# Kernel optimization log

Hardware: AMD Instinct MI355X
Metric: run time of the kernel (lower is better)

Reference implementation:

```python
import jax, jax.numpy as jnp
import numpy as np

N = 50000; F = 128; H = 128; E = 800000; G = 512; C = 1000; CE = 64; L = 128
EPS = 1e-5

def gcn_conv(x, src, dst, W, b, num_nodes):
    # PyG GCNConv: add self loops, sym-normalize, aggregate at dst
    loop = jnp.arange(num_nodes)
    s = jnp.concatenate([src, loop])
    d = jnp.concatenate([dst, loop])
    deg = jax.ops.segment_sum(jnp.ones_like(d, dtype=x.dtype), d, num_segments=num_nodes)
    dinv = jnp.where(deg > 0, jax.lax.rsqrt(deg), 0.0)
    norm = dinv[s] * dinv[d]                      # [E+N]
    h = x @ W                                     # [N,H]
    msg = h[s] * norm[:, None]                    # gather + scale
    return jax.ops.segment_sum(msg, d, num_segments=num_nodes) + b

def layer_norm(x, w, b):
    mu = jnp.mean(x, axis=-1, keepdims=True)
    var = jnp.var(x, axis=-1, keepdims=True)
    return (x - mu) * jax.lax.rsqrt(var + EPS) * w + b

def setup_inputs() -> dict:
    key = jax.random.key(0)
    ks = jax.random.split(key, 16)
    x = jax.random.normal(ks[0], (N, F), dtype=jnp.float32)
    edge_index = jax.random.randint(ks[1], (2, E), 0, N)
    batch = jnp.sort(jax.random.randint(ks[2], (N,), 0, G))
    cell_lines = jax.random.randint(ks[3], (G,), 0, C)
    def kai(k, shape):
        fan_in = shape[0]
        bound = np.sqrt(6.0 / fan_in)
        return jax.random.uniform(k, shape, jnp.float32, -bound, bound)
    return {
        'x': x, 'edge_index': edge_index, 'batch': batch, 'cell_lines': cell_lines,
        'W1': kai(ks[4], (F, H)), 'b1': jnp.zeros((H,), jnp.float32),
        'W2': kai(ks[5], (H, H)), 'b2': jnp.zeros((H,), jnp.float32),
        'emb': jax.random.normal(ks[6], (C, CE), dtype=jnp.float32),
        'Wc': kai(ks[7], (H + CE, H)), 'bc': jnp.zeros((H,), jnp.float32),
        'lnc_w': jnp.ones((H,), jnp.float32), 'lnc_b': jnp.zeros((H,), jnp.float32),
        'Wf1': kai(ks[8], (H, H)), 'bf1': jnp.zeros((H,), jnp.float32),
        'ln1_w': jnp.ones((H,), jnp.float32), 'ln1_b': jnp.zeros((H,), jnp.float32),
        'Wf2': kai(ks[9], (H, L)), 'bf2': jnp.zeros((L,), jnp.float32),
    }

def reference(x, edge_index, batch, cell_lines, W1, b1, W2, b2, emb, Wc, bc,
              lnc_w, lnc_b, Wf1, bf1, ln1_w, ln1_b, Wf2, bf2):
    src, dst = edge_index[0], edge_index[1]
    h = jax.nn.relu(gcn_conv(x, src, dst, W1, b1, N))
    h = jax.nn.relu(gcn_conv(h, src, dst, W2, b2, N))
    g = jax.ops.segment_sum(h, batch, num_segments=G)          # global_add_pool [G,H]
    ce = emb[cell_lines]                                       # [G,CE]
    comb = jnp.concatenate([g, ce], axis=1)
    comb = jax.nn.relu(layer_norm(comb @ Wc + bc, lnc_w, lnc_b))
    out = jax.nn.relu(comb @ Wf1 + bf1)                        # dropout = identity (eval)
    out = layer_norm(out, ln1_w, ln1_b)
    return out @ Wf2 + bf2
```

## Files before the change

### kernel.cpp

```cpp
#include <hip/hip_runtime.h>

#define N_NODES 50000
#define NFEAT 128
#define NEDGE 800000
#define NGRAPH 512
#define NCE 64
#define EPS 1e-5f
#define NBUCK 196
#define EPB 4096
#define BCAP 6144

typedef short s8v __attribute__((ext_vector_type(8)));
typedef float f4v __attribute__((ext_vector_type(4)));
typedef float f2v __attribute__((ext_vector_type(2)));

static __device__ __forceinline__ unsigned short f2bf(float f) {
    unsigned int u = __float_as_uint(f);
    unsigned int r = u + 0x7fffu + ((u >> 16) & 1u);
    return (unsigned short)(r >> 16);
}
static __device__ __forceinline__ float bf_lo(unsigned int packed) {
    return __uint_as_float(packed << 16);
}
static __device__ __forceinline__ float bf_hi(unsigned int packed) {
    return __uint_as_float(packed & 0xffff0000u);
}
static __device__ __forceinline__ float bf_us(unsigned short us) {
    return __uint_as_float(((unsigned int)us) << 16);
}
static __device__ __forceinline__ f2v unpk(unsigned int u) {
    f2v r; r.x = bf_lo(u); r.y = bf_hi(u); return r;
}
static __device__ __forceinline__ int swz(int row, int col) {
    return col ^ ((row & 7) << 3);
}

__global__ __launch_bounds__(256) void scatter_wcast_kernel(
    const int* __restrict__ ei, int* __restrict__ bucketCursor,
    unsigned int* __restrict__ recbuf, int E,
    const float* __restrict__ W1, const float* __restrict__ W2,
    unsigned short* __restrict__ WT1, unsigned short* __restrict__ WT2)
{
    __shared__ int hist[NBUCK];
    __shared__ int lbase[NBUCK];
    __shared__ int gbase[NBUCK];
    __shared__ int cur[NBUCK];
    __shared__ int scanbuf[256];
    __shared__ unsigned int staging[EPB];
    int tid = threadIdx.x;

    if (blockIdx.x >= NBUCK) {
        int b = blockIdx.x - NBUCK;
        const float* W = (b >= 64) ? W2 : W1;
        unsigned short* WT = (b >= 64) ? WT2 : WT1;
        int idx = (b & 63) * 256 + tid;
        int k = idx >> 7, n2 = idx & 127;
        WT[n2 * 128 + k] = f2bf(W[idx]);
        return;
    }

    if (tid < NBUCK) { hist[tid] = 0; cur[tid] = 0; }
    __syncthreads();

    unsigned int rec[EPB / 256];
    int e0 = blockIdx.x * EPB + tid;
#pragma unroll
    for (int i = 0; i < EPB / 256; ++i) {
        int e = e0 + i * 256;
        if (e < E) {
            unsigned int sv = (unsigned)ei[e];
            unsigned int dv = (unsigned)ei[E + e];
            rec[i] = sv | (dv << 16);
            atomicAdd(&hist[dv >> 8], 1);
        } else {
            rec[i] = 0xffffffffu;
        }
    }
    __syncthreads();
    int v = (tid < NBUCK) ? hist[tid] : 0;
    scanbuf[tid] = v; __syncthreads();
    for (int off = 1; off < 256; off <<= 1) {
        int t = (tid >= off) ? scanbuf[tid - off] : 0;
        __syncthreads();
        scanbuf[tid] += t;
        __syncthreads();
    }
    if (tid < NBUCK) lbase[tid] = scanbuf[tid] - v;
    int total = scanbuf[255];
    if (tid < NBUCK) gbase[tid] = (v > 0) ? atomicAdd(&bucketCursor[tid], v) : 0;
    __syncthreads();
#pragma unroll
    for (int i = 0; i < EPB / 256; ++i) {
        if (rec[i] != 0xffffffffu) {
            int b = rec[i] >> 24;
            int loc = atomicAdd(&cur[b], 1);
            staging[lbase[b] + loc] = rec[i];
        }
    }
    __syncthreads();
    for (int s = tid; s < total; s += 256) {
        unsigned int r = staging[s];
        int b = r >> 24;
        int pos = gbase[b] + (s - lbase[b]);
        if (pos < BCAP) recbuf[(size_t)b * BCAP + pos] = r;
    }
}

__global__ __launch_bounds__(256) void bucket_csr_kernel(
    const unsigned int* __restrict__ recbuf, const int* __restrict__ bucketCursor,
    int* __restrict__ rowbeg, unsigned short* __restrict__ deg,
    float* __restrict__ dinv, unsigned short* __restrict__ colidx)
{
    __shared__ int cnt[256];
    __shared__ int cur[256];
    __shared__ int scanbuf[256];
    __shared__ unsigned short stage[BCAP];
    int b = blockIdx.x, tid = threadIdx.x;
    int base = b * BCAP;
    int len = bucketCursor[b]; if (len > BCAP) len = BCAP;
    cnt[tid] = 0;
    __syncthreads();
    for (int s = tid; s < len; s += 256) {
        unsigned int r = recbuf[base + s];
        atomicAdd(&cnt[(r >> 16) & 255], 1);
    }
    __syncthreads();
    int v = cnt[tid];
    scanbuf[tid] = v; __syncthreads();
    for (int off = 1; off < 256; off <<= 1) {
        int t = (tid >= off) ? scanbuf[tid - off] : 0;
        __syncthreads();
        scanbuf[tid] += t;
        __syncthreads();
    }
    int excl = scanbuf[tid] - v;
    int node = b * 256 + tid;
    if (node < N_NODES) {
        rowbeg[node] = base + excl;
        deg[node] = (unsigned short)v;
        dinv[node] = rsqrtf((float)v + 1.0f);
    }
    cur[tid] = excl;
    __syncthreads();
    for (int s = tid; s < len; s += 256) {
        unsigned int r = recbuf[base + s];
        int pos = atomicAdd(&cur[(r >> 16) & 255], 1);
        stage[pos] = (unsigned short)(r & 0xffffu);
    }
    __syncthreads();
    for (int s = tid; s < len; s += 256) colidx[base + s] = stage[s];
}

template<bool FP32IN>
__global__ __launch_bounds__(256) void gemm_mfma_kernel(
    const void* __restrict__ Ain, const unsigned short* __restrict__ WTg,
    const float* __restrict__ dinv, unsigned short* __restrict__ HS, int nrows)
{
    __shared__ unsigned short as[128 * 128];
    __shared__ unsigned short wt[128 * 128];
    const int tid = threadIdx.x;
    const int row0 = blockIdx.x * 128;

    {
        const uint4* src = reinterpret_cast<const uint4*>(WTg);
        uint4* dst = reinterpret_cast<uint4*>(wt);
#pragma unroll
        for (int i = 0; i < 8; ++i) {
            int t = tid + i * 256;
            int d = (t & ~15) | ((t & 15) ^ ((t >> 4) & 7));
            dst[d] = src[t];
        }
    }
    if (FP32IN) {
        const float* X = (const float*)Ain;
#pragma unroll
        for (int i = 0; i < 16; ++i) {
            int f = tid + i * 256;
            int r = f >> 5, c4 = f & 31;
            int rr = row0 + r; if (rr >= nrows) rr = nrows - 1;
            float4 v = *reinterpret_cast<const float4*>(&X[rr * 128 + c4 * 4]);
            ushort4 o;
            o.x = f2bf(v.x); o.y = f2bf(v.y); o.z = f2bf(v.z); o.w = f2bf(v.w);
            *reinterpret_cast<ushort4*>(&as[r * 128 + swz(r, c4 * 4)]) = o;
        }
    } else {
        const unsigned short* X = (const unsigned short*)Ain;
#pragma unroll
        for (int i = 0; i < 8; ++i) {
            int f = tid + i * 256;
            int r = f >> 4, c8 = f & 15;
            int rr = row0 + r; if (rr >= nrows) rr = nrows - 1;
            *reinterpret_cast<uint4*>(&as[r * 128 + swz(r, c8 * 8)]) =
                *reinterpret_cast<const uint4*>(&X[rr * 128 + c8 * 8]);
        }
    }
    __syncthreads();

    const int w = tid >> 6;
    const int lane = tid & 63;
    const int quad = lane >> 4;
    const int col0 = lane & 15;

    s8v afr[2][4];
#pragma unroll
    for (int rt = 0; rt < 2; ++rt)
#pragma unroll
        for (int kt = 0; kt < 4; ++kt) {
            int rA = w * 32 + rt * 16 + col0;
            afr[rt][kt] = *reinterpret_cast<const s8v*>(
                &as[rA * 128 + swz(rA, kt * 32 + quad * 8)]);
        }

    f4v acc[2][8];
#pragma unroll
    for (int rt = 0; rt < 2; ++rt)
#pragma unroll
        for (int nt = 0; nt < 8; ++nt)
            acc[rt][nt] = (f4v){0.f, 0.f, 0.f, 0.f};

#pragma unroll
    for (int nt = 0; nt < 8; ++nt) {
        s8v bfr[4];
#pragma unroll
        for (int kt = 0; kt < 4; ++kt) {
            int rB = nt * 16 + col0;
            bfr[kt] = *reinterpret_cast<const s8v*>(
                &wt[rB * 128 + swz(rB, kt * 32 + quad * 8)]);
        }
#pragma unroll
        for (int rt = 0; rt < 2; ++rt)
#pragma unroll
            for (int kt = 0; kt < 4; ++kt)
                acc[rt][nt] = __builtin_amdgcn_mfma_f32_16x16x32_bf16(
                    afr[rt][kt], bfr[kt], acc[rt][nt], 0, 0, 0);
    }

    float dv[2][4];
#pragma unroll
    for (int rt = 0; rt < 2; ++rt)
#pragma unroll
        for (int reg = 0; reg < 4; ++reg) {
            int r = row0 + w * 32 + rt * 16 + quad * 4 + reg;
            dv[rt][reg] = (r < nrows) ? dinv[r] : 0.f;
        }

#pragma unroll
    for (int rt = 0; rt < 2; ++rt)
#pragma unroll
        for (int nt = 0; nt < 8; ++nt)
#pragma unroll
            for (int reg = 0; reg < 4; ++reg) {
                int rl = w * 32 + rt * 16 + quad * 4 + reg;
                as[rl * 128 + swz(rl, nt * 16 + col0)] = f2bf(acc[rt][nt][reg] * dv[rt][reg]);
            }
    __syncthreads();
#pragma unroll
    for (int i = 0; i < 8; ++i) {
        int f = tid + i * 256;
        int r = f >> 4, c8 = f & 15;
        if (row0 + r < nrows)
            *reinterpret_cast<uint4*>(&HS[(size_t)(row0 + r) * 128 + c8 * 8]) =
                *reinterpret_cast<const uint4*>(&as[r * 128 + swz(r, c8 * 8)]);
    }
}

static __device__ __forceinline__ uint2 agg_node(
    const uint2* __restrict__ H2, const int* __restrict__ rowbeg,
    const unsigned short* __restrict__ deg, const unsigned short* __restrict__ colidx,
    const float* __restrict__ dinv, const float* __restrict__ bias,
    int node, int lane)
{
    const int half = lane >> 5;
    const int sub = lane & 31;
    const int beg = rowbeg[node];
    const int cnt = (int)deg[node] + 1;
    f2v a01 = {0.f, 0.f}, a23 = {0.f, 0.f};
    f2v b01 = {0.f, 0.f}, b23 = {0.f, 0.f};
    for (int base = 0; base < cnt; base += 64) {
        int m = cnt - base; if (m > 64) m = 64;
        int p = base + lane;
        int idx = 0;
        if (lane < m) idx = (p == 0) ? node : (int)colidx[beg + p - 1];
        int j = 0;
        for (; j + 16 <= m; j += 16) {
            uint2 t[8];
#pragma unroll
            for (int q = 0; q < 8; ++q) {
                int u = __shfl(idx, j + q * 2 + half);
                t[q] = H2[(size_t)u * 32 + sub];
            }
#pragma unroll
            for (int q = 0; q < 8; q += 2) {
                a01 += unpk(t[q].x);     a23 += unpk(t[q].y);
                b01 += unpk(t[q + 1].x); b23 += unpk(t[q + 1].y);
            }
        }
        for (; j + 4 <= m; j += 4) {
            int ua = __shfl(idx, j + half);
            int ub = __shfl(idx, j + 2 + half);
            uint2 ta = H2[(size_t)ua * 32 + sub];
            uint2 tb = H2[(size_t)ub * 32 + sub];
            a01 += unpk(ta.x); a23 += unpk(ta.y);
            b01 += unpk(tb.x); b23 += unpk(tb.y);
        }
        if (j + 2 <= m) {
            int u = __shfl(idx, j + half);
            uint2 t = H2[(size_t)u * 32 + sub];
            a01 += unpk(t.x); a23 += unpk(t.y);
            j += 2;
        }
        if (j < m) {
            int u = __shfl(idx, j);
            uint2 t; t.x = 0u; t.y = 0u;
            if (half == 0) t = H2[(size_t)u * 32 + sub];
            a01 += unpk(t.x); a23 += unpk(t.y);
        }
    }
    a01 += b01; a23 += b23;
    float s0 = a01.x + __shfl_xor(a01.x, 32);
    float s1 = a01.y + __shfl_xor(a01.y, 32);
    float s2 = a23.x + __shfl_xor(a23.x, 32);
    float s3 = a23.y + __shfl_xor(a23.y, 32);
    float sc = dinv[node];
    float4 bv = *reinterpret_cast<const float4*>(&bias[sub * 4]);
    float o0 = fmaxf(fmaf(s0, sc, bv.x), 0.f);
    float o1 = fmaxf(fmaf(s1, sc, bv.y), 0.f);
    float o2 = fmaxf(fmaf(s2, sc, bv.z), 0.f);
    float o3 = fmaxf(fmaf(s3, sc, bv.w), 0.f);
    uint2 o;
    o.x = (unsigned int)f2bf(o0) | ((unsigned int)f2bf(o1) << 16);
    o.y = (unsigned int)f2bf(o2) | ((unsigned int)f2bf(o3) << 16);
    return o;
}

__global__ __launch_bounds__(1024, 8) void fused_agg_gemm_kernel(
    const uint2* __restrict__ H2, const int* __restrict__ rowbeg,
    const unsigned short* __restrict__ deg, const unsigned short* __restrict__ colidx,
    const float* __restrict__ dinv, const float* __restrict__ bias,
    const unsigned short* __restrict__ WTg, unsigned short* __restrict__ HS2, int n)
{
    __shared__ unsigned short as[128 * 128];
    __shared__ unsigned short wt[128 * 128];
    __shared__ int nodeCur;
    const int tid = threadIdx.x;
    const int row0 = blockIdx.x * 128;

    if (tid == 0) nodeCur = 0;
    {
        const uint4* src = reinterpret_cast<const uint4*>(WTg);
        uint4* dst = reinterpret_cast<uint4*>(wt);
        int t0 = tid, t1 = tid + 1024;
        dst[(t0 & ~15) | ((t0 & 15) ^ ((t0 >> 4) & 7))] = src[t0];
        dst[(t1 & ~15) | ((t1 & 15) ^ ((t1 >> 4) & 7))] = src[t1];
    }
    __syncthreads();

    const int w16 = tid >> 6;
    const int lane = tid & 63;

    uint2* asu2 = reinterpret_cast<uint2*>(as);
    for (;;) {
        int rr = 0;
        if (lane == 0) rr = atomicAdd(&nodeCur, 1);
        rr = __shfl(rr, 0);
        if (rr >= 128) break;
        int node = row0 + rr;
        if (node < n) {
            uint2 o = agg_node(H2, rowbeg, deg, colidx, dinv, bias, node, lane);
            if ((lane >> 5) == 0) {
                int sub = lane & 31;
                asu2[rr * 32 + (sub ^ ((rr & 7) << 1))] = o;
            }
        }
    }
    __syncthreads();

    const int quad = lane >> 4;
    const int col0 = lane & 15;
    const int wr  = w16 >> 1;
    const int nt0 = (w16 & 1) * 4;

    s8v afr[4];
#pragma unroll
    for (int kt = 0; kt < 4; ++kt) {
        int rA = wr * 16 + col0;
        afr[kt] = *reinterpret_cast<const s8v*>(
            &as[rA * 128 + swz(rA, kt * 32 + quad * 8)]);
    }

    f4v acc[4];
#pragma unroll
    for (int nt = 0; nt < 4; ++nt) acc[nt] = (f4v){0.f, 0.f, 0.f, 0.f};

#pragma unroll
    for (int nt = 0; nt < 4; ++nt) {
        s8v bfr[4];
#pragma unroll
        for (int kt = 0; kt < 4; ++kt) {
            int rB = (nt0 + nt) * 16 + col0;
            bfr[kt] = *reinterpret_cast<const s8v*>(
                &wt[rB * 128 + swz(rB, kt * 32 + quad * 8)]);
        }
#pragma unroll
        for (int kt = 0; kt < 4; ++kt)
            acc[nt] = __builtin_amdgcn_mfma_f32_16x16x32_bf16(
                afr[kt], bfr[kt], acc[nt], 0, 0, 0);
    }

    float dv[4];
#pragma unroll
    for (int reg = 0; reg < 4; ++reg) {
        int r = row0 + wr * 16 + quad * 4 + reg;
        dv[reg] = (r < n) ? dinv[r] : 0.f;
    }
    __syncthreads();
#pragma unroll
    for (int nt = 0; nt < 4; ++nt)
#pragma unroll
        for (int reg = 0; reg < 4; ++reg) {
            int rl = wr * 16 + quad * 4 + reg;
            as[rl * 128 + swz(rl, (nt0 + nt) * 16 + col0)] = f2bf(acc[nt][reg] * dv[reg]);
        }
    __syncthreads();
#pragma unroll
    for (int i = 0; i < 2; ++i) {
        int f = tid + i * 1024;
        int r = f >> 4, c8 = f & 15;
        if (row0 + r < n)
            *reinterpret_cast<uint4*>(&HS2[(size_t)(row0 + r) * 128 + c8 * 8]) =
                *reinterpret_cast<const uint4*>(&as[r * 128 + swz(r, c8 * 8)]);
    }
}

__global__ __launch_bounds__(1024, 8) void agg_pool_kernel(
    const uint2* __restrict__ H2, const int* __restrict__ rowbeg,
    const unsigned short* __restrict__ deg, const unsigned short* __restrict__ colidx,
    const float* __restrict__ dinv, const float* __restrict__ bias,
    const int* __restrict__ batch, float* __restrict__ pooled, int n)
{
    __shared__ unsigned short as[128 * 128];
    __shared__ int bsh[128];
    __shared__ float psum[8][132];
    __shared__ int nodeCur;
    const int tid = threadIdx.x;
    const int row0 = blockIdx.x * 128;
    if (tid == 0) nodeCur = 0;
    if (tid < 128) bsh[tid] = (row0 + tid < n) ? batch[row0 + tid] : -1;
    __syncthreads();

    const int lane = tid & 63;
    uint2* asu2 = reinterpret_cast<uint2*>(as);
    for (;;) {
        int rr = 0;
        if (lane == 0) rr = atomicAdd(&nodeCur, 1);
        rr = __shfl(rr, 0);
        if (rr >= 128) break;
        int node = row0 + rr;
        if (node < n) {
            uint2 o = agg_node(H2, rowbeg, deg, colidx, dinv, bias, node, lane);
            if ((lane >> 5) == 0) asu2[rr * 32 + (lane & 31)] = o;
        }
    }
    __syncthreads();

    const int g0 = bsh[0];
    int last = row0 + 127; if (last > n - 1) last = n - 1;
    const int g1 = batch[last];
    const int s = tid >> 7;
    const int f = tid & 127;
    for (int g = g0; g <= g1; ++g) {
        float acc = 0.f;
        for (int r = s; r < 128; r += 8)
            if (bsh[r] == g) acc += bf_us(as[r * 128 + f]);
        psum[s][f] = acc;
        __syncthreads();
        if (tid < 128) {
            float tot = 0.f;
#pragma unroll
            for (int q = 0; q < 8; ++q) tot += psum[q][f];
            atomicAdd(&pooled[g * 128 + f], tot);
        }
        __syncthreads();
    }
}

__global__ __launch_bounds__(256) void tail_kernel(
    const float* __restrict__ pooled,
    const int* __restrict__ cell, const float* __restrict__ emb,
    const float* __restrict__ Wc, const float* __restrict__ bc,
    const float* __restrict__ lncw, const float* __restrict__ lncb,
    const float* __restrict__ Wf1, const float* __restrict__ bf1,
    const float* __restrict__ ln1w, const float* __restrict__ ln1b,
    const float* __restrict__ Wf2, const float* __restrict__ bf2,
    float* __restrict__ out)
{
    __shared__ __align__(16) float comb[192];
    __shared__ __align__(16) float part[8][132];
    __shared__ float red[4];
    __shared__ __align__(16) float vec[128];
    const int gi = blockIdx.x;
    const int tid = threadIdx.x;
    const int cg = tid & 31;
    const int ks = tid >> 5;

    if (tid < 128) comb[tid] = pooled[gi * 128 + tid];
    else if (tid < 192) comb[tid] = emb[cell[gi] * 64 + (tid - 128)];
    __syncthreads();

    {
        float c[24];
#pragma unroll
        for (int i = 0; i < 6; ++i) {
            float4 t = *reinterpret_cast<const float4*>(&comb[ks * 24 + i * 4]);
            c[i * 4 + 0] = t.x; c[i * 4 + 1] = t.y; c[i * 4 + 2] = t.z; c[i * 4 + 3] = t.w;
        }
        float a0 = 0.f, a1 = 0.f, a2 = 0.f, a3 = 0.f;
#pragma unroll
        for (int i = 0; i < 24; ++i) {
            const float4 w = *reinterpret_cast<const float4*>(&Wc[(ks * 24 + i) * 128 + cg * 4]);
            a0 = fmaf(c[i], w.x, a0);
            a1 = fmaf(c[i], w.y, a1);
            a2 = fmaf(c[i], w.z, a2);
            a3 = fmaf(c[i], w.w, a3);
        }
        float4 o; o.x = a0; o.y = a1; o.z = a2; o.w = a3;
        *reinterpret_cast<float4*>(&part[ks][cg * 4]) = o;
    }
    __syncthreads();
    {
        float y = 0.f;
        if (tid < 128) {
            y = bc[tid];
#pragma unroll
            for (int s = 0; s < 8; ++s) y += part[s][tid];
        }
        float s1 = (tid < 128) ? y : 0.f;
        float s2 = (tid < 128) ? y * y : 0.f;
        if (tid < 128) {
#pragma unroll
            for (int off = 32; off > 0; off >>= 1) {
                s1 += __shfl_down(s1, off);
                s2 += __shfl_down(s2, off);
            }
            if ((tid & 63) == 0) { red[(tid >> 6) * 2] = s1; red[(tid >> 6) * 2 + 1] = s2; }
        }
        __syncthreads();
        float mu = (red[0] + red[2]) * (1.f / 128.f);
        float ms = (red[1] + red[3]) * (1.f / 128.f);
        float var = ms - mu * mu;
        if (tid < 128) {
            float yv = (y - mu) * rsqrtf(var + EPS) * lncw[tid] + lncb[tid];
            vec[tid] = fmaxf(yv, 0.f);
        }
    }
    __syncthreads();

    {
        float c[16];
#pragma unroll
        for (int i = 0; i < 4; ++i) {
            float4 t = *reinterpret_cast<const float4*>(&vec[ks * 16 + i * 4]);
            c[i * 4 + 0] = t.x; c[i * 4 + 1] = t.y; c[i * 4 + 2] = t.z; c[i * 4 + 3] = t.w;
        }
        float a0 = 0.f, a1 = 0.f, a2 = 0.f, a3 = 0.f;
#pragma unroll
        for (int i = 0; i < 16; ++i) {
            const float4 w = *reinterpret_cast<const float4*>(&Wf1[(ks * 16 + i) * 128 + cg * 4]);
            a0 = fmaf(c[i], w.x, a0);
            a1 = fmaf(c[i], w.y, a1);
            a2 = fmaf(c[i], w.z, a2);
            a3 = fmaf(c[i], w.w, a3);
        }
        float4 o; o.x = a0; o.y = a1; o.z = a2; o.w = a3;
        *reinterpret_cast<float4*>(&part[ks][cg * 4]) = o;
    }
    __syncthreads();
    {
        float y = 0.f;
        if (tid < 128) {
            y = bf1[tid];
#pragma unroll
            for (int s = 0; s < 8; ++s) y += part[s][tid];
            y = fmaxf(y, 0.f);
        }
        float s1 = (tid < 128) ? y : 0.f;
        float s2 = (tid < 128) ? y * y : 0.f;
        if (tid < 128) {
#pragma unroll
            for (int off = 32; off > 0; off >>= 1) {
                s1 += __shfl_down(s1, off);
                s2 += __shfl_down(s2, off);
            }
            if ((tid & 63) == 0) { red[(tid >> 6) * 2] = s1; red[(tid >> 6) * 2 + 1] = s2; }
        }
        __syncthreads();
        float mu = (red[0] + red[2]) * (1.f / 128.f);
        float ms = (red[1] + red[3]) * (1.f / 128.f);
        float var = ms - mu * mu;
        if (tid < 128)
            vec[tid] = (y - mu) * rsqrtf(var + EPS) * ln1w[tid] + ln1b[tid];
    }
    __syncthreads();

    {
        float c[16];
#pragma unroll
        for (int i = 0; i < 4; ++i) {
            float4 t = *reinterpret_cast<const float4*>(&vec[ks * 16 + i * 4]);
            c[i * 4 + 0] = t.x; c[i * 4 + 1] = t.y; c[i * 4 + 2] = t.z; c[i * 4 + 3] = t.w;
        }
        float a0 = 0.f, a1 = 0.f, a2 = 0.f, a3 = 0.f;
#pragma unroll
        for (int i = 0; i < 16; ++i) {
            const float4 w = *reinterpret_cast<const float4*>(&Wf2[(ks * 16 + i) * 128 + cg * 4]);
            a0 = fmaf(c[i], w.x, a0);
            a1 = fmaf(c[i], w.y, a1);
            a2 = fmaf(c[i], w.z, a2);
            a3 = fmaf(c[i], w.w, a3);
        }
        float4 o; o.x = a0; o.y = a1; o.z = a2; o.w = a3;
        *reinterpret_cast<float4*>(&part[ks][cg * 4]) = o;
    }
    __syncthreads();
    if (tid < 128) {
        float y = bf2[tid];
#pragma unroll
        for (int s = 0; s < 8; ++s) y += part[s][tid];
        out[gi * 128 + tid] = y;
    }
}

extern "C" void kernel_launch(void* const* d_in, const int* in_sizes, int n_in,
                              void* d_out, int out_size, void* d_ws, size_t ws_size,
                              hipStream_t stream) {
    const float* x    = (const float*)d_in[0];
    const int*   ei   = (const int*)d_in[1];
    const int*   batch= (const int*)d_in[2];
    const int*   cell = (const int*)d_in[3];
    const float* W1   = (const float*)d_in[4];
    const float* b1   = (const float*)d_in[5];
    const float* W2   = (const float*)d_in[6];
    const float* b2   = (const float*)d_in[7];
    const float* emb  = (const float*)d_in[8];
    const float* Wc   = (const float*)d_in[9];
    const float* bc   = (const float*)d_in[10];
    const float* lncw = (const float*)d_in[11];
    const float* lncb = (const float*)d_in[12];
    const float* Wf1  = (const float*)d_in[13];
    const float* bf1  = (const float*)d_in[14];
    const float* ln1w = (const float*)d_in[15];
    const float* ln1b = (const float*)d_in[16];
    const float* Wf2  = (const float*)d_in[17];
    const float* bf2  = (const float*)d_in[18];
    float* out = (float*)d_out;

    char* ws = (char*)d_ws;
    size_t off = 0;
    auto alloc = [&](size_t bytes) { char* p = ws + off; off = (off + bytes + 255) & ~size_t(255); return p; };
    int*            bucketCursor= (int*)  alloc(1024);
    float*          pooled      = (float*)alloc((size_t)NGRAPH * 128 * 4);
    float*          dinv        = (float*)alloc(N_NODES * 4);
    int*            rowbeg      = (int*)  alloc(N_NODES * 4);
    unsigned short* deg         = (unsigned short*)alloc(N_NODES * 2);
    unsigned short* colidx      = (unsigned short*)alloc((size_t)NBUCK * BCAP * 2);
    unsigned int*   recbuf      = (unsigned int*)alloc((size_t)NBUCK * BCAP * 4);
    unsigned short* wt1         = (unsigned short*)alloc(128 * 128 * 2);
    unsigned short* wt2         = (unsigned short*)alloc(128 * 128 * 2);
    unsigned short* hs          = (unsigned short*)alloc((size_t)N_NODES * 128 * 2);
    unsigned short* hs2         = (unsigned short*)alloc((size_t)N_NODES * 128 * 2);

    const int nbEdge = (NEDGE + EPB - 1) / EPB;
    const int nbGemm = (N_NODES + 127) / 128;

    hipMemsetAsync(bucketCursor, 0, 1024 + (size_t)NGRAPH * 128 * 4, stream);

    scatter_wcast_kernel<<<nbEdge + 128, 256, 0, stream>>>(ei, bucketCursor, recbuf, NEDGE,
                                                           W1, W2, wt1, wt2);
    bucket_csr_kernel<<<NBUCK, 256, 0, stream>>>(recbuf, bucketCursor, rowbeg, deg, dinv, colidx);

    gemm_mfma_kernel<true><<<nbGemm, 256, 0, stream>>>(x, wt1, dinv, hs, N_NODES);

    fused_agg_gemm_kernel<<<nbGemm, 1024, 0, stream>>>(
        (const uint2*)hs, rowbeg, deg, colidx, dinv, b1, wt2, hs2, N_NODES);

    agg_pool_kernel<<<nbGemm, 1024, 0, stream>>>(
        (const uint2*)hs2, rowbeg, deg, colidx, dinv, b2, batch, pooled, N_NODES);

    tail_kernel<<<NGRAPH, 256, 0, stream>>>(pooled, cell, emb, Wc, bc, lncw, lncb,
                                            Wf1, bf1, ln1w, ln1b, Wf2, bf2, out);
}
```

Before: 212.8 us.

## Merge edge scatter and first GEMM into one launch, move dinv scaling into aggregation

Result: no change. 215.5 us (+1.2%).

```diff
diff --git a/kernel.cpp b/kernel.cpp
--- a/kernel.cpp
+++ b/kernel.cpp
@@ -35,74 +35,177 @@
     return col ^ ((row & 7) << 3);
 }
 
-__global__ __launch_bounds__(256) void scatter_wcast_kernel(
+struct ScatterSmem {
+    int hist[NBUCK]; int lbase[NBUCK]; int gbase[NBUCK]; int cur[NBUCK];
+    int scanbuf[256];
+    unsigned int staging[EPB];
+};
+struct GemmSmem {
+    unsigned short as[128 * 128];
+    unsigned short wt[128 * 128];
+};
+
+__global__ __launch_bounds__(256) void mega_kernel(
     const int* __restrict__ ei, int* __restrict__ bucketCursor,
     unsigned int* __restrict__ recbuf, int E,
     const float* __restrict__ W1, const float* __restrict__ W2,
-    unsigned short* __restrict__ WT1, unsigned short* __restrict__ WT2)
+    unsigned short* __restrict__ WT2,
+    const float* __restrict__ x, unsigned short* __restrict__ HS, int nrows)
 {
-    __shared__ int hist[NBUCK];
-    __shared__ int lbase[NBUCK];
-    __shared__ int gbase[NBUCK];
-    __shared__ int cur[NBUCK];
-    __shared__ int scanbuf[256];
-    __shared__ unsigned int staging[EPB];
-    int tid = threadIdx.x;
-
-    if (blockIdx.x >= NBUCK) {
-        int b = blockIdx.x - NBUCK;
-        const float* W = (b >= 64) ? W2 : W1;
-        unsigned short* WT = (b >= 64) ? WT2 : WT1;
-        int idx = (b & 63) * 256 + tid;
+    __shared__ __align__(16) char smemraw[sizeof(GemmSmem)];
+    const int tid = threadIdx.x;
+    const int bid = blockIdx.x;
+
+    if (bid < NBUCK) {
+        ScatterSmem* sm = reinterpret_cast<ScatterSmem*>(smemraw);
+        if (tid < NBUCK) { sm->hist[tid] = 0; sm->cur[tid] = 0; }
+        __syncthreads();
+
+        unsigned int rec[EPB / 256];
+        int e0 = bid * EPB + tid;
+#pragma unroll
+        for (int i = 0; i < EPB / 256; ++i) {
+            int e = e0 + i * 256;
+            if (e < E) {
+                unsigned int sv = (unsigned)ei[e];
+                unsigned int dv = (unsigned)ei[E + e];
+                rec[i] = sv | (dv << 16);
+                atomicAdd(&sm->hist[dv >> 8], 1);
+            } else {
+                rec[i] = 0xffffffffu;
+            }
+        }
+        __syncthreads();
+        int v = (tid < NBUCK) ? sm->hist[tid] : 0;
+        sm->scanbuf[tid] = v; __syncthreads();
+        for (int off = 1; off < 256; off <<= 1) {
+            int t = (tid >= off) ? sm->scanbuf[tid - off] : 0;
+            __syncthreads();
+            sm->scanbuf[tid] += t;
+            __syncthreads();
+        }
+        if (tid < NBUCK) sm->lbase[tid] = sm->scanbuf[tid] - v;
+        int total = sm->scanbuf[255];
+        if (tid < NBUCK) sm->gbase[tid] = (v > 0) ? atomicAdd(&bucketCursor[tid], v) : 0;
+        __syncthreads();
+#pragma unroll
+        for (int i = 0; i < EPB / 256; ++i) {
+            if (rec[i] != 0xffffffffu) {
+                int b = rec[i] >> 24;
+                int loc = atomicAdd(&sm->cur[b], 1);
+                sm->staging[sm->lbase[b] + loc] = rec[i];
+            }
+        }
+        __syncthreads();
+        for (int s = tid; s < total; s += 256) {
+            unsigned int r = sm->staging[s];
+            int b = r >> 24;
+            int pos = sm->gbase[b] + (s - sm->lbase[b]);
+            if (pos < BCAP) recbuf[(size_t)b * BCAP + pos] = r;
+        }
+        return;
+    }
+
+    if (bid < NBUCK + 64) {
+        int b = bid - NBUCK;
+        int idx = b * 256 + tid;
         int k = idx >> 7, n2 = idx & 127;
-        WT[n2 * 128 + k] = f2bf(W[idx]);
+        WT2[n2 * 128 + k] = f2bf(W2[idx]);
         return;
     }
 
-    if (tid < NBUCK) { hist[tid] = 0; cur[tid] = 0; }
-    __syncthreads();
-
-    unsigned int rec[EPB / 256];
-    int e0 = blockIdx.x * EPB + tid;
-#pragma unroll
-    for (int i = 0; i < EPB / 256; ++i) {
-        int e = e0 + i * 256;
-        if (e < E) {
-            unsigned int sv = (unsigned)ei[e];
-            unsigned int dv = (unsigned)ei[E + e];
-            rec[i] = sv | (dv << 16);
-            atomicAdd(&hist[dv >> 8], 1);
-        } else {
-            rec[i] = 0xffffffffu;
-        }
-    }
-    __syncthreads();
-    int v = (tid < NBUCK) ? hist[tid] : 0;
-    scanbuf[tid] = v; __syncthreads();
-    for (int off = 1; off < 256; off <<= 1) {
-        int t = (tid >= off) ? scanbuf[tid - off] : 0;
-        __syncthreads();
-        scanbuf[tid] += t;
-        __syncthreads();
-    }
-    if (tid < NBUCK) lbase[tid] = scanbuf[tid] - v;
-    int total = scanbuf[255];
-    if (tid < NBUCK) gbase[tid] = (v > 0) ? atomicAdd(&bucketCursor[tid], v) : 0;
-    __syncthreads();
-#pragma unroll
-    for (int i = 0; i < EPB / 256; ++i) {
-        if (rec[i] != 0xffffffffu) {
-            int b = rec[i] >> 24;
-            int loc = atomicAdd(&cur[b], 1);
-            staging[lbase[b] + loc] = rec[i];
-        }
-    }
-    __syncthreads();
-    for (int s = tid; s < total; s += 256) {
-        unsigned int r = staging[s];
-        int b = r >> 24;
-        int pos = gbase[b] + (s - lbase[b]);
-        if (pos < BCAP) recbuf[(size_t)b * BCAP + pos] = r;
+    GemmSmem* gm = reinterpret_cast<GemmSmem*>(smemraw);
+    unsigned short* as = gm->as;
+    unsigned short* wt = gm->wt;
+    const int row0 = (bid - NBUCK - 64) * 128;
+
+#pragma unroll
+    for (int i = 0; i < 8; ++i) {
+        int flat = tid + i * 256;
+        int n = flat & 127;
+        int k0 = (flat >> 7) << 3;
+        ushort4 pa, pb;
+        pa.x = f2bf(W1[(k0 + 0) * 128 + n]);
+        pa.y = f2bf(W1[(k0 + 1) * 128 + n]);
+        pa.z = f2bf(W1[(k0 + 2) * 128 + n]);
+        pa.w = f2bf(W1[(k0 + 3) * 128 + n]);
+        pb.x = f2bf(W1[(k0 + 4) * 128 + n]);
+        pb.y = f2bf(W1[(k0 + 5) * 128 + n]);
+        pb.z = f2bf(W1[(k0 + 6) * 128 + n]);
+        pb.w = f2bf(W1[(k0 + 7) * 128 + n]);
+        int base = n * 128 + swz(n, k0);
+        *reinterpret_cast<ushort4*>(&wt[base]) = pa;
+        *reinterpret_cast<ushort4*>(&wt[base + 4]) = pb;
+    }
+#pragma unroll
+    for (int i = 0; i < 16; ++i) {
+        int f = tid + i * 256;
+        int r = f >> 5, c4 = f & 31;
+        int rr = row0 + r; if (rr >= nrows) rr = nrows - 1;
+        float4 v = *reinterpret_cast<const float4*>(&x[rr * 128 + c4 * 4]);
+        ushort4 o;
+        o.x = f2bf(v.x); o.y = f2bf(v.y); o.z = f2bf(v.z); o.w = f2bf(v.w);
+        *reinterpret_cast<ushort4*>(&as[r * 128 + swz(r, c4 * 4)]) = o;
+    }
+    __syncthreads();
+
+    const int w = tid >> 6;
+    const int lane = tid & 63;
+    const int quad = lane >> 4;
+    const int col0 = lane & 15;
+
+    s8v afr[2][4];
+#pragma unroll
+    for (int rt = 0; rt < 2; ++rt)
+#pragma unroll
+        for (int kt = 0; kt < 4; ++kt) {
+            int rA = w * 32 + rt * 16 + col0;
+            afr[rt][kt] = *reinterpret_cast<const s8v*>(
+                &as[rA * 128 + swz(rA, kt * 32 + quad * 8)]);
+        }
+
+    f4v acc[2][8];
+#pragma unroll
+    for (int rt = 0; rt < 2; ++rt)
+#pragma unroll
+        for (int nt = 0; nt < 8; ++nt)
+            acc[rt][nt] = (f4v){0.f, 0.f, 0.f, 0.f};
+
+#pragma unroll
+    for (int nt = 0; nt < 8; ++nt) {
+        s8v bfr[4];
+#pragma unroll
+        for (int kt = 0; kt < 4; ++kt) {
+            int rB = nt * 16 + col0;
+            bfr[kt] = *reinterpret_cast<const s8v*>(
+                &wt[rB * 128 + swz(rB, kt * 32 + quad * 8)]);
+        }
+#pragma unroll
+        for (int rt = 0; rt < 2; ++rt)
+#pragma unroll
+            for (int kt = 0; kt < 4; ++kt)
+                acc[rt][nt] = __builtin_amdgcn_mfma_f32_16x16x32_bf16(
+                    afr[rt][kt], bfr[kt], acc[rt][nt], 0, 0, 0);
+    }
+
+    __syncthreads();
+#pragma unroll
+    for (int rt = 0; rt < 2; ++rt)
+#pragma unroll
+        for (int nt = 0; nt < 8; ++nt)
+#pragma unroll
+            for (int reg = 0; reg < 4; ++reg) {
+                int rl = w * 32 + rt * 16 + quad * 4 + reg;
+                as[rl * 128 + swz(rl, nt * 16 + col0)] = f2bf(acc[rt][nt][reg]);
+            }
+    __syncthreads();
+#pragma unroll
+    for (int i = 0; i < 8; ++i) {
+        int f = tid + i * 256;
+        int r = f >> 4, c8 = f & 15;
+        if (row0 + r < nrows)
+            *reinterpret_cast<uint4*>(&HS[(size_t)(row0 + r) * 128 + c8 * 8]) =
+                *reinterpret_cast<const uint4*>(&as[r * 128 + swz(r, c8 * 8)]);
     }
 }
 
@@ -151,119 +254,7 @@
     for (int s = tid; s < len; s += 256) colidx[base + s] = stage[s];
 }
 
-template<bool FP32IN>
-__global__ __launch_bounds__(256) void gemm_mfma_kernel(
-    const void* __restrict__ Ain, const unsigned short* __restrict__ WTg,
-    const float* __restrict__ dinv, unsigned short* __restrict__ HS, int nrows)
-{
-    __shared__ unsigned short as[128 * 128];
-    __shared__ unsigned short wt[128 * 128];
-    const int tid = threadIdx.x;
-    const int row0 = blockIdx.x * 128;
-
-    {
-        const uint4* src = reinterpret_cast<const uint4*>(WTg);
-        uint4* dst = reinterpret_cast<uint4*>(wt);
-#pragma unroll
-        for (int i = 0; i < 8; ++i) {
-            int t = tid + i * 256;
-            int d = (t & ~15) | ((t & 15) ^ ((t >> 4) & 7));
-            dst[d] = src[t];
-        }
-    }
-    if (FP32IN) {
-        const float* X = (const float*)Ain;
-#pragma unroll
-        for (int i = 0; i < 16; ++i) {
-            int f = tid + i * 256;
-            int r = f >> 5, c4 = f & 31;
-            int rr = row0 + r; if (rr >= nrows) rr = nrows - 1;
-            float4 v = *reinterpret_cast<const float4*>(&X[rr * 128 + c4 * 4]);
-            ushort4 o;
-            o.x = f2bf(v.x); o.y = f2bf(v.y); o.z = f2bf(v.z); o.w = f2bf(v.w);
-            *reinterpret_cast<ushort4*>(&as[r * 128 + swz(r, c4 * 4)]) = o;
-        }
-    } else {
-        const unsigned short* X = (const unsigned short*)Ain;
-#pragma unroll
-        for (int i = 0; i < 8; ++i) {
-            int f = tid + i * 256;
-            int r = f >> 4, c8 = f & 15;
-            int rr = row0 + r; if (rr >= nrows) rr = nrows - 1;
-            *reinterpret_cast<uint4*>(&as[r * 128 + swz(r, c8 * 8)]) =
-                *reinterpret_cast<const uint4*>(&X[rr * 128 + c8 * 8]);
-        }
-    }
-    __syncthreads();
-
-    const int w = tid >> 6;
-    const int lane = tid & 63;
-    const int quad = lane >> 4;
-    const int col0 = lane & 15;
-
-    s8v afr[2][4];
-#pragma unroll
-    for (int rt = 0; rt < 2; ++rt)
-#pragma unroll
-        for (int kt = 0; kt < 4; ++kt) {
-            int rA = w * 32 + rt * 16 + col0;
-            afr[rt][kt] = *reinterpret_cast<const s8v*>(
-                &as[rA * 128 + swz(rA, kt * 32 + quad * 8)]);
-        }
-
-    f4v acc[2][8];
-#pragma unroll
-    for (int rt = 0; rt < 2; ++rt)
-#pragma unroll
-        for (int nt = 0; nt < 8; ++nt)
-            acc[rt][nt] = (f4v){0.f, 0.f, 0.f, 0.f};
-
-#pragma unroll
-    for (int nt = 0; nt < 8; ++nt) {
-        s8v bfr[4];
-#pragma unroll
-        for (int kt = 0; kt < 4; ++kt) {
-            int rB = nt * 16 + col0;
-            bfr[kt] = *reinterpret_cast<const s8v*>(
-                &wt[rB * 128 + swz(rB, kt * 32 + quad * 8)]);
-        }
-#pragma unroll
-        for (int rt = 0; rt < 2; ++rt)
-#pragma unroll
-            for (int kt = 0; kt < 4; ++kt)
-                acc[rt][nt] = __builtin_amdgcn_mfma_f32_16x16x32_bf16(
-                    afr[rt][kt], bfr[kt], acc[rt][nt], 0, 0, 0);
-    }
-
-    float dv[2][4];
-#pragma unroll
-    for (int rt = 0; rt < 2; ++rt)
-#pragma unroll
-        for (int reg = 0; reg < 4; ++reg) {
-            int r = row0 + w * 32 + rt * 16 + quad * 4 + reg;
-            dv[rt][reg] = (r < nrows) ? dinv[r] : 0.f;
-        }
-
-#pragma unroll
-    for (int rt = 0; rt < 2; ++rt)
-#pragma unroll
-        for (int nt = 0; nt < 8; ++nt)
-#pragma unroll
-            for (int reg = 0; reg < 4; ++reg) {
-                int rl = w * 32 + rt * 16 + quad * 4 + reg;
-                as[rl * 128 + swz(rl, nt * 16 + col0)] = f2bf(acc[rt][nt][reg] * dv[rt][reg]);
-            }
-    __syncthreads();
-#pragma unroll
-    for (int i = 0; i < 8; ++i) {
-        int f = tid + i * 256;
-        int r = f >> 4, c8 = f & 15;
-        if (row0 + r < nrows)
-            *reinterpret_cast<uint4*>(&HS[(size_t)(row0 + r) * 128 + c8 * 8]) =
-                *reinterpret_cast<const uint4*>(&as[r * 128 + swz(r, c8 * 8)]);
-    }
-}
-
+template<bool SC>
 static __device__ __forceinline__ uint2 agg_node(
     const uint2* __restrict__ H2, const int* __restrict__ rowbeg,
     const unsigned short* __restrict__ deg, const unsigned short* __restrict__ colidx,
@@ -280,40 +271,81 @@
         int m = cnt - base; if (m > 64) m = 64;
         int p = base + lane;
         int idx = 0;
-        if (lane < m) idx = (p == 0) ? node : (int)colidx[beg + p - 1];
+        float dvw = 0.f;
+        if (lane < m) {
+            idx = (p == 0) ? node : (int)colidx[beg + p - 1];
+            if (SC) dvw = dinv[idx];
+        }
         int j = 0;
         for (; j + 16 <= m; j += 16) {
             uint2 t[8];
+            float sc[8];
 #pragma unroll
             for (int q = 0; q < 8; ++q) {
-                int u = __shfl(idx, j + q * 2 + half);
+                int src = j + q * 2 + half;
+                int u = __shfl(idx, src);
+                if (SC) sc[q] = __shfl(dvw, src);
                 t[q] = H2[(size_t)u * 32 + sub];
             }
 #pragma unroll
             for (int q = 0; q < 8; q += 2) {
-                a01 += unpk(t[q].x);     a23 += unpk(t[q].y);
-                b01 += unpk(t[q + 1].x); b23 += unpk(t[q + 1].y);
+                if (SC) {
+                    f2v xa = unpk(t[q].x), ya = unpk(t[q].y);
+                    a01.x = fmaf(sc[q], xa.x, a01.x); a01.y = fmaf(sc[q], xa.y, a01.y);
+                    a23.x = fmaf(sc[q], ya.x, a23.x); a23.y = fmaf(sc[q], ya.y, a23.y);
+                    f2v xb = unpk(t[q + 1].x), yb = unpk(t[q + 1].y);
+                    b01.x = fmaf(sc[q + 1], xb.x, b01.x); b01.y = fmaf(sc[q + 1], xb.y, b01.y);
+                    b23.x = fmaf(sc[q + 1], yb.x, b23.x); b23.y = fmaf(sc[q + 1], yb.y, b23.y);
+                } else {
+                    a01 += unpk(t[q].x);     a23 += unpk(t[q].y);
+                    b01 += unpk(t[q + 1].x); b23 += unpk(t[q + 1].y);
+                }
             }
         }
         for (; j + 4 <= m; j += 4) {
             int ua = __shfl(idx, j + half);
             int ub = __shfl(idx, j + 2 + half);
+            float sa = SC ? __shfl(dvw, j + half) : 0.f;
+            float sb = SC ? __shfl(dvw, j + 2 + half) : 0.f;
             uint2 ta = H2[(size_t)ua * 32 + sub];
             uint2 tb = H2[(size_t)ub * 32 + sub];
-            a01 += unpk(ta.x); a23 += unpk(ta.y);
-            b01 += unpk(tb.x); b23 += unpk(tb.y);
+            if (SC) {
+                f2v xa = unpk(ta.x), ya = unpk(ta.y);
+                a01.x = fmaf(sa, xa.x, a01.x); a01.y = fmaf(sa, xa.y, a01.y);
+                a23.x = fmaf(sa, ya.x, a23.x); a23.y = fmaf(sa, ya.y, a23.y);
+                f2v xb = unpk(tb.x), yb = unpk(tb.y);
+                b01.x = fmaf(sb, xb.x, b01.x); b01.y = fmaf(sb, xb.y, b01.y);
+                b23.x = fmaf(sb, yb.x, b23.x); b23.y = fmaf(sb, yb.y, b23.y);
+            } else {
+                a01 += unpk(ta.x); a23 += unpk(ta.y);
+                b01 += unpk(tb.x); b23 += unpk(tb.y);
+            }
         }
         if (j + 2 <= m) {
             int u = __shfl(idx, j + half);
+            float sa = SC ? __shfl(dvw, j + half) : 0.f;
             uint2 t = H2[(size_t)u * 32 + sub];
-            a01 += unpk(t.x); a23 += unpk(t.y);
+            if (SC) {
+                f2v xa = unpk(t.x), ya = unpk(t.y);
+                a01.x = fmaf(sa, xa.x, a01.x); a01.y = fmaf(sa, xa.y, a01.y);
+                a23.x = fmaf(sa, ya.x, a23.x); a23.y = fmaf(sa, ya.y, a23.y);
+            } else {
+                a01 += unpk(t.x); a23 += unpk(t.y);
+            }
             j += 2;
         }
         if (j < m) {
             int u = __shfl(idx, j);
+            float sa = SC ? __shfl(dvw, j) : 0.f;
             uint2 t; t.x = 0u; t.y = 0u;
             if (half == 0) t = H2[(size_t)u * 32 + sub];
-            a01 += unpk(t.x); a23 += unpk(t.y);
+            if (SC) {
+                f2v xa = unpk(t.x), ya = unpk(t.y);
+                a01.x = fmaf(sa, xa.x, a01.x); a01.y = fmaf(sa, xa.y, a01.y);
+                a23.x = fmaf(sa, ya.x, a23.x); a23.y = fmaf(sa, ya.y, a23.y);
+            } else {
+                a01 += unpk(t.x); a23 += unpk(t.y);
+            }
         }
     }
     a01 += b01; a23 += b23;
@@ -321,12 +353,12 @@
     float s1 = a01.y + __shfl_xor(a01.y, 32);
     float s2 = a23.x + __shfl_xor(a23.x, 32);
     float s3 = a23.y + __shfl_xor(a23.y, 32);
-    float sc = dinv[node];
+    float scn = dinv[node];
     float4 bv = *reinterpret_cast<const float4*>(&bias[sub * 4]);
-    float o0 = fmaxf(fmaf(s0, sc, bv.x), 0.f);
-    float o1 = fmaxf(fmaf(s1, sc, bv.y), 0.f);
-    float o2 = fmaxf(fmaf(s2, sc, bv.z), 0.f);
-    float o3 = fmaxf(fmaf(s3, sc, bv.w), 0.f);
+    float o0 = fmaxf(fmaf(s0, scn, bv.x), 0.f);
+    float o1 = fmaxf(fmaf(s1, scn, bv.y), 0.f);
+    float o2 = fmaxf(fmaf(s2, scn, bv.z), 0.f);
+    float o3 = fmaxf(fmaf(s3, scn, bv.w), 0.f);
     uint2 o;
     o.x = (unsigned int)f2bf(o0) | ((unsigned int)f2bf(o1) << 16);
     o.y = (unsigned int)f2bf(o2) | ((unsigned int)f2bf(o3) << 16);
@@ -366,7 +398,7 @@
         if (rr >= 128) break;
         int node = row0 + rr;
         if (node < n) {
-            uint2 o = agg_node(H2, rowbeg, deg, colidx, dinv, bias, node, lane);
+            uint2 o = agg_node<true>(H2, rowbeg, deg, colidx, dinv, bias, node, lane);
             if ((lane >> 5) == 0) {
                 int sub = lane & 31;
                 asu2[rr * 32 + (sub ^ ((rr & 7) << 1))] = o;
@@ -457,7 +489,7 @@
         if (rr >= 128) break;
         int node = row0 + rr;
         if (node < n) {
-            uint2 o = agg_node(H2, rowbeg, deg, colidx, dinv, bias, node, lane);
+            uint2 o = agg_node<false>(H2, rowbeg, deg, colidx, dinv, bias, node, lane);
             if ((lane >> 5) == 0) asu2[rr * 32 + (lane & 31)] = o;
         }
     }
@@ -664,7 +696,6 @@
     unsigned short* deg         = (unsigned short*)alloc(N_NODES * 2);
     unsigned short* colidx      = (unsigned short*)alloc((size_t)NBUCK * BCAP * 2);
     unsigned int*   recbuf      = (unsigned int*)alloc((size_t)NBUCK * BCAP * 4);
-    unsigned short* wt1         = (unsigned short*)alloc(128 * 128 * 2);
     unsigned short* wt2         = (unsigned short*)alloc(128 * 128 * 2);
     unsigned short* hs          = (unsigned short*)alloc((size_t)N_NODES * 128 * 2);
     unsigned short* hs2         = (unsigned short*)alloc((size_t)N_NODES * 128 * 2);
@@ -674,11 +705,10 @@
 
     hipMemsetAsync(bucketCursor, 0, 1024 + (size_t)NGRAPH * 128 * 4, stream);
 
-    scatter_wcast_kernel<<<nbEdge + 128, 256, 0, stream>>>(ei, bucketCursor, recbuf, NEDGE,
-                                                           W1, W2, wt1, wt2);
+    mega_kernel<<<nbEdge + 64 + nbGemm, 256, 0, stream>>>(
+        ei, bucketCursor, recbuf, NEDGE, W1, W2, wt2, x, hs, N_NODES);
+
     bucket_csr_kernel<<<NBUCK, 256, 0, stream>>>(recbuf, bucketCursor, rowbeg, deg, dinv, colidx);
-
-    gemm_mfma_kernel<true><<<nbGemm, 256, 0, stream>>>(x, wt1, dinv, hs, N_NODES);
 
     fused_agg_gemm_kernel<<<nbGemm, 1024, 0, stream>>>(
         (const uint2*)hs, rowbeg, deg, colidx, dinv, b1, wt2, hs2, N_NODES);
```

## Store node features in 32-column chunks and gather one chunk at a time

Applied to the files above, without the earlier changes.

New measurement: 305.5 us. +43.6%, slower.

```diff
diff --git a/kernel.cpp b/kernel.cpp
--- a/kernel.cpp
+++ b/kernel.cpp
@@ -9,6 +9,8 @@
 #define NBUCK 196
 #define EPB 4096
 #define BCAP 6144
+#define CSTR_US (N_NODES * 32)
+#define CSTR_U32 (N_NODES * 16)
 
 typedef short s8v __attribute__((ext_vector_type(8)));
 typedef float f4v __attribute__((ext_vector_type(4)));
@@ -151,9 +153,8 @@
     for (int s = tid; s < len; s += 256) colidx[base + s] = stage[s];
 }
 
-template<bool FP32IN>
 __global__ __launch_bounds__(256) void gemm_mfma_kernel(
-    const void* __restrict__ Ain, const unsigned short* __restrict__ WTg,
+    const float* __restrict__ X, const unsigned short* __restrict__ WTg,
     const float* __restrict__ dinv, unsigned short* __restrict__ HS, int nrows)
 {
     __shared__ unsigned short as[128 * 128];
@@ -171,28 +172,15 @@
             dst[d] = src[t];
         }
     }
-    if (FP32IN) {
-        const float* X = (const float*)Ain;
-#pragma unroll
-        for (int i = 0; i < 16; ++i) {
-            int f = tid + i * 256;
-            int r = f >> 5, c4 = f & 31;
-            int rr = row0 + r; if (rr >= nrows) rr = nrows - 1;
-            float4 v = *reinterpret_cast<const float4*>(&X[rr * 128 + c4 * 4]);
-            ushort4 o;
-            o.x = f2bf(v.x); o.y = f2bf(v.y); o.z = f2bf(v.z); o.w = f2bf(v.w);
-            *reinterpret_cast<ushort4*>(&as[r * 128 + swz(r, c4 * 4)]) = o;
-        }
-    } else {
-        const unsigned short* X = (const unsigned short*)Ain;
-#pragma unroll
-        for (int i = 0; i < 8; ++i) {
-            int f = tid + i * 256;
-            int r = f >> 4, c8 = f & 15;
-            int rr = row0 + r; if (rr >= nrows) rr = nrows - 1;
-            *reinterpret_cast<uint4*>(&as[r * 128 + swz(r, c8 * 8)]) =
-                *reinterpret_cast<const uint4*>(&X[rr * 128 + c8 * 8]);
-        }
+#pragma unroll
+    for (int i = 0; i < 16; ++i) {
+        int f = tid + i * 256;
+        int r = f >> 5, c4 = f & 31;
+        int rr = row0 + r; if (rr >= nrows) rr = nrows - 1;
+        float4 v = *reinterpret_cast<const float4*>(&X[rr * 128 + c4 * 4]);
+        ushort4 o;
+        o.x = f2bf(v.x); o.y = f2bf(v.y); o.z = f2bf(v.z); o.w = f2bf(v.w);
+        *reinterpret_cast<ushort4*>(&as[r * 128 + swz(r, c4 * 4)]) = o;
     }
     __syncthreads();
 
@@ -258,94 +246,97 @@
     for (int i = 0; i < 8; ++i) {
         int f = tid + i * 256;
         int r = f >> 4, c8 = f & 15;
-        if (row0 + r < nrows)
-            *reinterpret_cast<uint4*>(&HS[(size_t)(row0 + r) * 128 + c8 * 8]) =
+        if (row0 + r < nrows) {
+            int ch = c8 >> 2, off = (c8 & 3) * 8;
+            *reinterpret_cast<uint4*>(
+                &HS[(size_t)ch * CSTR_US + (size_t)(row0 + r) * 32 + off]) =
                 *reinterpret_cast<const uint4*>(&as[r * 128 + swz(r, c8 * 8)]);
-    }
-}
-
-static __device__ __forceinline__ uint2 agg_node(
-    const uint2* __restrict__ H2, const int* __restrict__ rowbeg,
+        }
+    }
+}
+
+template<bool SWZ>
+static __device__ __forceinline__ void gather_tile_chunked(
+    const unsigned int* __restrict__ Hu, const int* __restrict__ rowbeg,
     const unsigned short* __restrict__ deg, const unsigned short* __restrict__ colidx,
     const float* __restrict__ dinv, const float* __restrict__ bias,
-    int node, int lane)
+    unsigned int* asu, int* nodeCur, int row0, int n, int tid)
 {
-    const int half = lane >> 5;
-    const int sub = lane & 31;
-    const int beg = rowbeg[node];
-    const int cnt = (int)deg[node] + 1;
-    f2v a01 = {0.f, 0.f}, a23 = {0.f, 0.f};
-    f2v b01 = {0.f, 0.f}, b23 = {0.f, 0.f};
-    for (int base = 0; base < cnt; base += 64) {
-        int m = cnt - base; if (m > 64) m = 64;
-        int p = base + lane;
-        int idx = 0;
-        if (lane < m) idx = (p == 0) ? node : (int)colidx[beg + p - 1];
-        int j = 0;
-        for (; j + 16 <= m; j += 16) {
-            uint2 t[8];
-#pragma unroll
-            for (int q = 0; q < 8; ++q) {
-                int u = __shfl(idx, j + q * 2 + half);
-                t[q] = H2[(size_t)u * 32 + sub];
+    const int lane = tid & 63;
+    const int g = lane >> 4;
+    const int s16 = lane & 15;
+#pragma unroll 1
+    for (int c = 0; c < 4; ++c) {
+        const unsigned int* T = Hu + (size_t)c * CSTR_U32;
+        const float2 bv = *reinterpret_cast<const float2*>(&bias[c * 32 + s16 * 2]);
+        for (;;) {
+            int rr = 0;
+            if (lane == 0) rr = atomicAdd(&nodeCur[c], 1);
+            rr = __shfl(rr, 0);
+            if (rr >= 128) break;
+            int node = row0 + rr;
+            if (node >= n) continue;
+            int beg = rowbeg[node];
+            int cnt = (int)deg[node] + 1;
+            f2v acc = {0.f, 0.f};
+            for (int base = 0; base < cnt; base += 64) {
+                int m = cnt - base; if (m > 64) m = 64;
+                int p = base + lane;
+                int idx = 0;
+                if (lane < m) idx = (p == 0) ? node : (int)colidx[beg + p - 1];
+                int j = 0;
+                for (; j + 16 <= m; j += 16) {
+                    unsigned int t[4];
+#pragma unroll
+                    for (int q = 0; q < 4; ++q) {
+                        int u = __shfl(idx, j + q * 4 + g);
+                        t[q] = T[(size_t)u * 16 + s16];
+                    }
+#pragma unroll
+                    for (int q = 0; q < 4; ++q) acc += unpk(t[q]);
+                }
+                for (; j + 4 <= m; j += 4) {
+                    int u = __shfl(idx, j + g);
+                    acc += unpk(T[(size_t)u * 16 + s16]);
+                }
+                if (j < m) {
+                    int srcl = j + g;
+                    bool act = srcl < m;
+                    int u = __shfl(idx, act ? srcl : j);
+                    unsigned int t = 0;
+                    if (act) t = T[(size_t)u * 16 + s16];
+                    acc += unpk(t);
+                }
             }
-#pragma unroll
-            for (int q = 0; q < 8; q += 2) {
-                a01 += unpk(t[q].x);     a23 += unpk(t[q].y);
-                b01 += unpk(t[q + 1].x); b23 += unpk(t[q + 1].y);
+            acc.x += __shfl_xor(acc.x, 16); acc.y += __shfl_xor(acc.y, 16);
+            acc.x += __shfl_xor(acc.x, 32); acc.y += __shfl_xor(acc.y, 32);
+            if (lane < 16) {
+                float sc = dinv[node];
+                float o0 = fmaxf(fmaf(acc.x, sc, bv.x), 0.f);
+                float o1 = fmaxf(fmaf(acc.y, sc, bv.y), 0.f);
+                unsigned int pk = (unsigned int)f2bf(o0) | ((unsigned int)f2bf(o1) << 16);
+                int col = c * 32 + s16 * 2;
+                int us = SWZ ? (rr * 128 + swz(rr, col)) : (rr * 128 + col);
+                asu[us >> 1] = pk;
             }
         }
-        for (; j + 4 <= m; j += 4) {
-            int ua = __shfl(idx, j + half);
-            int ub = __shfl(idx, j + 2 + half);
-            uint2 ta = H2[(size_t)ua * 32 + sub];
-            uint2 tb = H2[(size_t)ub * 32 + sub];
-            a01 += unpk(ta.x); a23 += unpk(ta.y);
-            b01 += unpk(tb.x); b23 += unpk(tb.y);
-        }
-        if (j + 2 <= m) {
-            int u = __shfl(idx, j + half);
-            uint2 t = H2[(size_t)u * 32 + sub];
-            a01 += unpk(t.x); a23 += unpk(t.y);
-            j += 2;
-        }
-        if (j < m) {
-            int u = __shfl(idx, j);
-            uint2 t; t.x = 0u; t.y = 0u;
-            if (half == 0) t = H2[(size_t)u * 32 + sub];
-            a01 += unpk(t.x); a23 += unpk(t.y);
-        }
-    }
-    a01 += b01; a23 += b23;
-    float s0 = a01.x + __shfl_xor(a01.x, 32);
-    float s1 = a01.y + __shfl_xor(a01.y, 32);
-    float s2 = a23.x + __shfl_xor(a23.x, 32);
-    float s3 = a23.y + __shfl_xor(a23.y, 32);
-    float sc = dinv[node];
-    float4 bv = *reinterpret_cast<const float4*>(&bias[sub * 4]);
-    float o0 = fmaxf(fmaf(s0, sc, bv.x), 0.f);
-    float o1 = fmaxf(fmaf(s1, sc, bv.y), 0.f);
-    float o2 = fmaxf(fmaf(s2, sc, bv.z), 0.f);
-    float o3 = fmaxf(fmaf(s3, sc, bv.w), 0.f);
-    uint2 o;
-    o.x = (unsigned int)f2bf(o0) | ((unsigned int)f2bf(o1) << 16);
-    o.y = (unsigned int)f2bf(o2) | ((unsigned int)f2bf(o3) << 16);
-    return o;
+        __syncthreads();
+    }
 }
 
 __global__ __launch_bounds__(1024, 8) void fused_agg_gemm_kernel(
-    const uint2* __restrict__ H2, const int* __restrict__ rowbeg,
+    const unsigned int* __restrict__ Hu, const int* __restrict__ rowbeg,
     const unsigned short* __restrict__ deg, const unsigned short* __restrict__ colidx,
     const float* __restrict__ dinv, const float* __restrict__ bias,
     const unsigned short* __restrict__ WTg, unsigned short* __restrict__ HS2, int n)
 {
     __shared__ unsigned short as[128 * 128];
     __shared__ unsigned short wt[128 * 128];
-    __shared__ int nodeCur;
+    __shared__ int nodeCur[4];
     const int tid = threadIdx.x;
     const int row0 = blockIdx.x * 128;
 
-    if (tid == 0) nodeCur = 0;
+    if (tid < 4) nodeCur[tid] = 0;
     {
         const uint4* src = reinterpret_cast<const uint4*>(WTg);
         uint4* dst = reinterpret_cast<uint4*>(wt);
@@ -355,26 +346,11 @@
     }
     __syncthreads();
 
+    gather_tile_chunked<true>(Hu, rowbeg, deg, colidx, dinv, bias,
+                              reinterpret_cast<unsigned int*>(as), nodeCur, row0, n, tid);
+
     const int w16 = tid >> 6;
     const int lane = tid & 63;
-
-    uint2* asu2 = reinterpret_cast<uint2*>(as);
-    for (;;) {
-        int rr = 0;
-        if (lane == 0) rr = atomicAdd(&nodeCur, 1);
-        rr = __shfl(rr, 0);
-        if (rr >= 128) break;
-        int node = row0 + rr;
-        if (node < n) {
-            uint2 o = agg_node(H2, rowbeg, deg, colidx, dinv, bias, node, lane);
-            if ((lane >> 5) == 0) {
-                int sub = lane & 31;
-                asu2[rr * 32 + (sub ^ ((rr & 7) << 1))] = o;
-            }
-        }
-    }
-    __syncthreads();
-
     const int quad = lane >> 4;
     const int col0 = lane & 15;
     const int wr  = w16 >> 1;
@@ -426,14 +402,17 @@
     for (int i = 0; i < 2; ++i) {
         int f = tid + i * 1024;
         int r = f >> 4, c8 = f & 15;
-        if (row0 + r < n)
-            *reinterpret_cast<uint4*>(&HS2[(size_t)(row0 + r) * 128 + c8 * 8]) =
+        if (row0 + r < n) {
+            int ch = c8 >> 2, off = (c8 & 3) * 8;
+            *reinterpret_cast<uint4*>(
+                &HS2[(size_t)ch * CSTR_US + (size_t)(row0 + r) * 32 + off]) =
                 *reinterpret_cast<const uint4*>(&as[r * 128 + swz(r, c8 * 8)]);
+        }
     }
 }
 
 __global__ __launch_bounds__(1024, 8) void agg_pool_kernel(
-    const uint2* __restrict__ H2, const int* __restrict__ rowbeg,
+    const unsigned int* __restrict__ Hu, const int* __restrict__ rowbeg,
     const unsigned short* __restrict__ deg, const unsigned short* __restrict__ colidx,
     const float* __restrict__ dinv, const float* __restrict__ bias,
     const int* __restrict__ batch, float* __restrict__ pooled, int n)
@@ -441,27 +420,15 @@
     __shared__ unsigned short as[128 * 128];
     __shared__ int bsh[128];
     __shared__ float psum[8][132];
-    __shared__ int nodeCur;
+    __shared__ int nodeCur[4];
     const int tid = threadIdx.x;
     const int row0 = blockIdx.x * 128;
-    if (tid == 0) nodeCur = 0;
+    if (tid < 4) nodeCur[tid] = 0;
     if (tid < 128) bsh[tid] = (row0 + tid < n) ? batch[row0 + tid] : -1;
     __syncthreads();
 
-    const int lane = tid & 63;
-    uint2* asu2 = reinterpret_cast<uint2*>(as);
-    for (;;) {
-        int rr = 0;
-        if (lane == 0) rr = atomicAdd(&nodeCur, 1);
-        rr = __shfl(rr, 0);
-        if (rr >= 128) break;
-        int node = row0 + rr;
-        if (node < n) {
-            uint2 o = agg_node(H2, rowbeg, deg, colidx, dinv, bias, node, lane);
-            if ((lane >> 5) == 0) asu2[rr * 32 + (lane & 31)] = o;
-        }
-    }
-    __syncthreads();
+    gather_tile_chunked<false>(Hu, rowbeg, deg, colidx, dinv, bias,
+                               reinterpret_cast<unsigned int*>(as), nodeCur, row0, n, tid);
 
     const int g0 = bsh[0];
     int last = row0 + 127; if (last > n - 1) last = n - 1;
@@ -678,13 +645,13 @@
                                                            W1, W2, wt1, wt2);
     bucket_csr_kernel<<<NBUCK, 256, 0, stream>>>(recbuf, bucketCursor, rowbeg, deg, dinv, colidx);
 
-    gemm_mfma_kernel<true><<<nbGemm, 256, 0, stream>>>(x, wt1, dinv, hs, N_NODES);
+    gemm_mfma_kernel<<<nbGemm, 256, 0, stream>>>(x, wt1, dinv, hs, N_NODES);
 
     fused_agg_gemm_kernel<<<nbGemm, 1024, 0, stream>>>(
-        (const uint2*)hs, rowbeg, deg, colidx, dinv, b1, wt2, hs2, N_NODES);
+        (const unsigned int*)hs, rowbeg, deg, colidx, dinv, b1, wt2, hs2, N_NODES);
 
     agg_pool_kernel<<<nbGemm, 1024, 0, stream>>>(
-        (const uint2*)hs2, rowbeg, deg, colidx, dinv, b2, batch, pooled, N_NODES);
+        (const unsigned int*)hs2, rowbeg, deg, colidx, dinv, b2, batch, pooled, N_NODES);
 
     tail_kernel<<<NGRAPH, 256, 0, stream>>>(pooled, cell, emb, Wc, bc, lncw, lncb,
                                             Wf1, bf1, ln1w, ln1b, Wf2, bf2, out);
```
